# Optimization experiments

Hardware: AMD Instinct MI355X
Metric: run time of the kernel (lower is better)

## Reference

```python
import jax, jax.numpy as jnp
import numpy as np

B, C, VC, H, W = 4, 256, 128, 64, 64


def setup_inputs() -> dict:
    key = jax.random.key(0)
    kx, kq, kk, kv = jax.random.split(key, 4)
    # Conv2d 1x1 no-bias weights are just [out_channels, in_channels] matrices.
    s = 1.0 / np.sqrt(C)
    return {
        "x": jax.random.normal(kx, (B, C, H, W), dtype=jnp.float32),
        "Wq": jax.random.uniform(kq, (VC, C), minval=-s, maxval=s, dtype=jnp.float32),
        "Wk": jax.random.uniform(kk, (VC, C), minval=-s, maxval=s, dtype=jnp.float32),
        "Wv": jax.random.uniform(kv, (VC, C), minval=-s, maxval=s, dtype=jnp.float32),
    }


def reference(x, Wq, Wk, Wv):
    # 1x1 convs == per-pixel channel GEMMs
    Q = jnp.einsum('bchw,dc->bdhw', x, Wq)  # [B, VC, H, W]
    K = jnp.einsum('bchw,dc->bdhw', x, Wk)
    V = jnp.einsum('bchw,dc->bdhw', x, Wv)
    b, d, h, w = Q.shape
    # affinity over all spatial pairs: [B, H, W, H, W]
    aff = jnp.einsum('bdij,bdkl->bijkl', Q, K).reshape(b, h, w, h * w)
    aff = jax.nn.softmax(aff, axis=3).reshape(b, h, w, h, w)
    # attention-weighted aggregation of values
    out = jnp.einsum('bijkl,bdkl->bdij', aff, V)  # [B, VC, H, W]
    return out
```

## Files before the change

kernel.cpp:

```cpp
#include <hip/hip_runtime.h>
#include <hip/hip_bf16.h>

#define B_ 4
#define C_ 256
#define D_ 128
#define N_ 4096

typedef float f32x4 __attribute__((ext_vector_type(4)));
typedef short bf16x8 __attribute__((ext_vector_type(8)));
typedef short s16x4 __attribute__((ext_vector_type(4)));
typedef unsigned short u16;
typedef unsigned int u32;

__device__ __forceinline__ u16 f2bf(float f) {
  unsigned u = __float_as_uint(f);
  u += 0x7fffu + ((u >> 16) & 1u);
  return (u16)(u >> 16);
}
__device__ __forceinline__ float bf2f(u16 v) {
  return __uint_as_float(((u32)v) << 16);
}
__device__ __forceinline__ u32 cvt_pk_bf16(float a, float b) {
  u32 r;
  asm("v_cvt_pk_bf16_f32 %0, %1, %2" : "=v"(r) : "v"(a), "v"(b));
  return r;
}

__global__ __launch_bounds__(256) void castw_kernel(
    const float* __restrict__ Wq, const float* __restrict__ Wk,
    const float* __restrict__ Wv, u16* __restrict__ Whi,
    u16* __restrict__ Wlo) {
  const int i = blockIdx.x * 256 + threadIdx.x;
  const int m = i >> 13;
  const int j = (i & 8191) * 4;
  const float* src = (m == 0) ? Wq : (m == 1) ? Wk : Wv;
  const float scale = (m == 0) ? 1.44269504f : 1.0f;
  const float4 v = *(const float4*)(src + j);
  const float vv[4] = {v.x * scale, v.y * scale, v.z * scale, v.w * scale};
  s16x4 h, l;
#pragma unroll
  for (int k = 0; k < 4; ++k) {
    const u16 hb = f2bf(vv[k]);
    h[k] = (short)hb;
    l[k] = (short)f2bf(vv[k] - bf2f(hb));
  }
  *(s16x4*)&Whi[m * 32768 + j] = h;
  *(s16x4*)&Wlo[m * 32768 + j] = l;
}

__global__ __launch_bounds__(256, 2) void proj_kernel(
    const float* __restrict__ x, const u16* __restrict__ Whi,
    const u16* __restrict__ Wlo, u16* __restrict__ Qo, u16* __restrict__ Ko,
    u16* __restrict__ Vt) {
  __shared__ __align__(16) u16 xs_h[32 * 256];
  __shared__ __align__(16) u16 xs_l[32 * 256];

  const int n0 = blockIdx.x * 32;
  const int b = blockIdx.y;
  const int t = threadIdx.x;
  const int w = t >> 6, lane = t & 63, g = lane >> 4, c = lane & 15;

  {
    const float* xb = x + ((size_t)b * C_) * N_ + n0;
#pragma unroll
    for (int r = 0; r < 8; ++r) {
      const int id = r * 256 + t;
      const int cr = id >> 3, nq = (id & 7) * 4;
      const float4 v = *(const float4*)(xb + (size_t)cr * N_ + nq);
      const float vv[4] = {v.x, v.y, v.z, v.w};
#pragma unroll
      for (int k2 = 0; k2 < 4; ++k2) {
        const int idx2 = (nq + k2) * 256 + (cr ^ (((nq + k2) & 7) << 3));
        const u16 hb = f2bf(vv[k2]);
        xs_h[idx2] = hb;
        xs_l[idx2] = f2bf(vv[k2] - bf2f(hb));
      }
    }
  }
  __syncthreads();

  if (w < 2) {
    const size_t wo = (size_t)w * 32768;
    u16* __restrict__ O = (w == 0 ? Qo : Ko) + (size_t)b * N_ * D_;
#pragma unroll 1
    for (int dt = 0; dt < 8; ++dt) {
      bf16x8 wfh[8], wfl[8];
#pragma unroll
      for (int kc = 0; kc < 8; ++kc) {
        const size_t off = wo + (size_t)(dt * 16 + c) * 256 + kc * 32 + g * 8;
        wfh[kc] = *(const bf16x8*)&Whi[off];
        wfl[kc] = *(const bf16x8*)&Wlo[off];
      }
#pragma unroll
      for (int nt = 0; nt < 2; ++nt) {
        f32x4 a = {0.f, 0.f, 0.f, 0.f};
#pragma unroll
        for (int kc = 0; kc < 8; ++kc) {
          const int xi = (nt * 16 + c) * 256 +
                         ((kc * 32 + g * 8) ^ ((c & 7) << 3));
          const bf16x8 xh = *(const bf16x8*)&xs_h[xi];
          const bf16x8 xl = *(const bf16x8*)&xs_l[xi];
          a = __builtin_amdgcn_mfma_f32_16x16x32_bf16(xh, wfh[kc], a, 0, 0, 0);
          a = __builtin_amdgcn_mfma_f32_16x16x32_bf16(xh, wfl[kc], a, 0, 0, 0);
          a = __builtin_amdgcn_mfma_f32_16x16x32_bf16(xl, wfh[kc], a, 0, 0, 0);
        }
#pragma unroll
        for (int i = 0; i < 4; ++i)
          O[(size_t)(n0 + nt * 16 + g * 4 + i) * D_ + dt * 16 + c] = f2bf(a[i]);
      }
    }
  } else {
    const size_t wo = (size_t)2 * 32768;
    const int d0 = (w - 2) * 64;
    u16* __restrict__ O = Vt + (size_t)b * D_ * N_;
#pragma unroll 1
    for (int dt = 0; dt < 4; ++dt) {
      bf16x8 wfh[8], wfl[8];
#pragma unroll
      for (int kc = 0; kc < 8; ++kc) {
        const size_t off =
            wo + (size_t)(d0 + dt * 16 + c) * 256 + kc * 32 + g * 8;
        wfh[kc] = *(const bf16x8*)&Whi[off];
        wfl[kc] = *(const bf16x8*)&Wlo[off];
      }
#pragma unroll
      for (int nt = 0; nt < 2; ++nt) {
        f32x4 a = {0.f, 0.f, 0.f, 0.f};
#pragma unroll
        for (int kc = 0; kc < 8; ++kc) {
          const int xi = (nt * 16 + c) * 256 +
                         ((kc * 32 + g * 8) ^ ((c & 7) << 3));
          const bf16x8 xh = *(const bf16x8*)&xs_h[xi];
          const bf16x8 xl = *(const bf16x8*)&xs_l[xi];
          a = __builtin_amdgcn_mfma_f32_16x16x32_bf16(wfh[kc], xh, a, 0, 0, 0);
          a = __builtin_amdgcn_mfma_f32_16x16x32_bf16(wfl[kc], xh, a, 0, 0, 0);
          a = __builtin_amdgcn_mfma_f32_16x16x32_bf16(wfh[kc], xl, a, 0, 0, 0);
        }
#pragma unroll
        for (int i = 0; i < 4; ++i)
          O[(size_t)(d0 + dt * 16 + g * 4 + i) * N_ + n0 + nt * 16 + c] =
              f2bf(a[i]);
      }
    }
  }
}

__device__ __forceinline__ int kIdx(int row, int col) {
  return row * 128 + (col ^ ((row & 7) << 3));
}
__device__ __forceinline__ int vIdx(int d, int col) {
  return d * 64 + (col ^ ((d & 7) << 3));
}
__device__ __forceinline__ int pIdx(int q, int col) {
  return q * 64 + (col ^ ((q & 7) << 3));
}

__global__ __launch_bounds__(256, 2) void attn_kernel(
    const u16* __restrict__ Q, const u16* __restrict__ K,
    const u16* __restrict__ Vt, u16* __restrict__ op,
    float* __restrict__ mb, float* __restrict__ lb,
    float* __restrict__ outf, int qt, int rem) {
  __shared__ __align__(16) u16 lds_k[64 * 128];
  __shared__ __align__(16) u16 lds_vt[128 * 64];
  __shared__ __align__(16) u16 lds_p[4][32 * 64];

  const int b = blockIdx.y;
  const int sid = blockIdx.z;
  const int q0 = blockIdx.x * 128;
  const int NT = qt + (sid < rem ? 1 : 0);
  const int t0 = sid * qt + (sid < rem ? sid : rem);
  const int k0 = t0 * 64;
  const int t = threadIdx.x;
  const int w = t >> 6, lane = t & 63, g = lane >> 4, c = lane & 15;
  const int qw = q0 + w * 32;

  const u16* __restrict__ Qb = Q + (size_t)b * N_ * D_;
  const u16* __restrict__ Kb = K + (size_t)b * N_ * D_;
  const u16* __restrict__ Vb = Vt + (size_t)b * D_ * N_;

  bf16x8 qf[2][4];
#pragma unroll
  for (int qh = 0; qh < 2; ++qh)
#pragma unroll
    for (int kc = 0; kc < 4; ++kc)
      qf[qh][kc] =
          *(const bf16x8*)&Qb[(size_t)(qw + qh * 16 + c) * D_ + kc * 32 + g * 8];

  f32x4 acc[8][2];
#pragma unroll
  for (int dt = 0; dt < 8; ++dt)
#pragma unroll
    for (int qh = 0; qh < 2; ++qh) acc[dt][qh] = (f32x4){0.f, 0.f, 0.f, 0.f};
  float mrow[2] = {-3.0e38f, -3.0e38f};
  float lrow[2] = {0.f, 0.f};
  const float THR = 11.5415603f;

  bf16x8 krg[4], vrg[4];
  auto load_tile = [&](int kbase) {
#pragma unroll
    for (int i = 0; i < 4; ++i) {
      const int idx = i * 256 + t;
      krg[i] = *(const bf16x8*)&Kb[(size_t)(kbase + (idx >> 4)) * D_ + (idx & 15) * 8];
      vrg[i] = *(const bf16x8*)&Vb[(size_t)(idx >> 3) * N_ + kbase + (idx & 7) * 8];
    }
  };
  load_tile(k0);

  u16* __restrict__ pw = lds_p[w];

  for (int kt = 0; kt < NT; ++kt) {
    __syncthreads();
#pragma unroll
    for (int i = 0; i < 4; ++i) {
      const int idx = i * 256 + t;
      *(bf16x8*)&lds_k[kIdx(idx >> 4, (idx & 15) * 8)] = krg[i];
      *(bf16x8*)&lds_vt[vIdx(idx >> 3, (idx & 7) * 8)] = vrg[i];
    }
    if (kt + 1 < NT) load_tile(k0 + (kt + 1) * 64);
    __syncthreads();

    f32x4 s[4][2];
#pragma unroll
    for (int ct = 0; ct < 4; ++ct)
#pragma unroll
      for (int qh = 0; qh < 2; ++qh) s[ct][qh] = (f32x4){0.f, 0.f, 0.f, 0.f};
    __builtin_amdgcn_s_setprio(1);
#pragma unroll
    for (int kc = 0; kc < 4; ++kc) {
#pragma unroll
      for (int ct = 0; ct < 4; ++ct) {
        const bf16x8 kf =
            *(const bf16x8*)&lds_k[kIdx(ct * 16 + c, kc * 32 + g * 8)];
        s[ct][0] = __builtin_amdgcn_mfma_f32_16x16x32_bf16(kf, qf[0][kc], s[ct][0], 0, 0, 0);
        s[ct][1] = __builtin_amdgcn_mfma_f32_16x16x32_bf16(kf, qf[1][kc], s[ct][1], 0, 0, 0);
      }
    }
    __builtin_amdgcn_s_setprio(0);

    float pm[2];
#pragma unroll
    for (int qh = 0; qh < 2; ++qh) {
      const float m0 = fmaxf(fmaxf(s[0][qh][0], s[0][qh][1]),
                             fmaxf(s[0][qh][2], s[0][qh][3]));
      const float m1 = fmaxf(fmaxf(s[1][qh][0], s[1][qh][1]),
                             fmaxf(s[1][qh][2], s[1][qh][3]));
      const float m2 = fmaxf(fmaxf(s[2][qh][0], s[2][qh][1]),
                             fmaxf(s[2][qh][2], s[2][qh][3]));
      const float m3 = fmaxf(fmaxf(s[3][qh][0], s[3][qh][1]),
                             fmaxf(s[3][qh][2], s[3][qh][3]));
      float p = fmaxf(fmaxf(m0, m1), fmaxf(m2, m3));
      p = fmaxf(p, __shfl_xor(p, 16));
      p = fmaxf(p, __shfl_xor(p, 32));
      pm[qh] = p;
    }
    const bool need =
        __any((pm[0] > mrow[0] + THR) || (pm[1] > mrow[1] + THR));
    if (need) {
#pragma unroll
      for (int qh = 0; qh < 2; ++qh) {
        const float mnew = fmaxf(mrow[qh], pm[qh]);
        const float scl = exp2f(mrow[qh] - mnew);
        lrow[qh] *= scl;
        mrow[qh] = mnew;
#pragma unroll
        for (int dt = 0; dt < 8; ++dt) {
          acc[dt][qh][0] *= scl; acc[dt][qh][1] *= scl;
          acc[dt][qh][2] *= scl; acc[dt][qh][3] *= scl;
        }
      }
    }
#pragma unroll
    for (int qh = 0; qh < 2; ++qh) {
      float rs = 0.f;
#pragma unroll
      for (int ct = 0; ct < 4; ++ct)
#pragma unroll
        for (int i = 0; i < 4; ++i) {
          const float p = exp2f(s[ct][qh][i] - mrow[qh]);
          s[ct][qh][i] = p;
          rs += p;
        }
      rs += __shfl_xor(rs, 16);
      rs += __shfl_xor(rs, 32);
      lrow[qh] += rs;
    }

#pragma unroll
    for (int qh = 0; qh < 2; ++qh)
#pragma unroll
      for (int ct = 0; ct < 4; ++ct) {
        const int pi = pIdx(qh * 16 + c, ct * 16 + g * 4);
        union { u32 w2[2]; s16x4 v; } pu;
        pu.w2[0] = cvt_pk_bf16(s[ct][qh][0], s[ct][qh][1]);
        pu.w2[1] = cvt_pk_bf16(s[ct][qh][2], s[ct][qh][3]);
        *(s16x4*)&pw[pi] = pu.v;
      }
    asm volatile("" ::: "memory");

    __builtin_amdgcn_s_setprio(1);
#pragma unroll
    for (int kc = 0; kc < 2; ++kc) {
      const bf16x8 pf0 = *(const bf16x8*)&pw[pIdx(c, kc * 32 + g * 8)];
      const bf16x8 pf1 = *(const bf16x8*)&pw[pIdx(16 + c, kc * 32 + g * 8)];
#pragma unroll
      for (int dt = 0; dt < 8; ++dt) {
        const bf16x8 vf =
            *(const bf16x8*)&lds_vt[vIdx(dt * 16 + c, kc * 32 + g * 8)];
        acc[dt][0] = __builtin_amdgcn_mfma_f32_16x16x32_bf16(vf, pf0, acc[dt][0], 0, 0, 0);
        acc[dt][1] = __builtin_amdgcn_mfma_f32_16x16x32_bf16(vf, pf1, acc[dt][1], 0, 0, 0);
      }
    }
    __builtin_amdgcn_s_setprio(0);
  }

#pragma unroll
  for (int qh = 0; qh < 2; ++qh) {
    const int n = qw + qh * 16 + c;
    if (mb) {
      u16* __restrict__ ob = op + ((size_t)(sid * B_ + b) * D_) * N_;
#pragma unroll
      for (int dt = 0; dt < 8; ++dt)
#pragma unroll
        for (int i = 0; i < 4; ++i)
          ob[(size_t)(dt * 16 + g * 4 + i) * N_ + n] = f2bf(acc[dt][qh][i]);
      if (g == 0) {
        mb[(size_t)(sid * B_ + b) * N_ + n] = mrow[qh];
        lb[(size_t)(sid * B_ + b) * N_ + n] = lrow[qh];
      }
    } else {
      const float linv = 1.0f / lrow[qh];
      float* __restrict__ ob = outf + (size_t)b * D_ * N_;
#pragma unroll
      for (int dt = 0; dt < 8; ++dt)
#pragma unroll
        for (int i = 0; i < 4; ++i)
          ob[(size_t)(dt * 16 + g * 4 + i) * N_ + n] = acc[dt][qh][i] * linv;
    }
  }
}

__global__ __launch_bounds__(256) void combine_kernel(
    const u16* __restrict__ op, const float* __restrict__ mbu,
    const float* __restrict__ lbu, float* __restrict__ out, int S) {
  const int idx = blockIdx.x * 256 + threadIdx.x;
  const int n0 = (idx & (N_ / 4 - 1)) * 4;
  const int bd = idx >> 10;
  const int b = bd >> 7, d = bd & (D_ - 1);

  float4 msv[8], lsv[8];
  float M0 = -3e38f, M1 = -3e38f, M2 = -3e38f, M3 = -3e38f;
#pragma unroll
  for (int s = 0; s < 8; ++s)
    if (s < S) {
      msv[s] = *(const float4*)&mbu[(size_t)(s * B_ + b) * N_ + n0];
      lsv[s] = *(const float4*)&lbu[(size_t)(s * B_ + b) * N_ + n0];
      M0 = fmaxf(M0, msv[s].x); M1 = fmaxf(M1, msv[s].y);
      M2 = fmaxf(M2, msv[s].z); M3 = fmaxf(M3, msv[s].w);
    }
  float d0 = 0.f, d1 = 0.f, d2 = 0.f, d3 = 0.f;
  float a0 = 0.f, a1 = 0.f, a2 = 0.f, a3 = 0.f;
#pragma unroll
  for (int s = 0; s < 8; ++s)
    if (s < S) {
      const float w0 = exp2f(msv[s].x - M0);
      const float w1 = exp2f(msv[s].y - M1);
      const float w2 = exp2f(msv[s].z - M2);
      const float w3 = exp2f(msv[s].w - M3);
      d0 += lsv[s].x * w0; d1 += lsv[s].y * w1;
      d2 += lsv[s].z * w2; d3 += lsv[s].w * w3;
      const s16x4 o =
          *(const s16x4*)&op[((size_t)(s * B_ + b) * D_ + d) * N_ + n0];
      a0 += w0 * bf2f((u16)o[0]); a1 += w1 * bf2f((u16)o[1]);
      a2 += w2 * bf2f((u16)o[2]); a3 += w3 * bf2f((u16)o[3]);
    }
  float4 r = {a0 / d0, a1 / d1, a2 / d2, a3 / d3};
  *(float4*)&out[((size_t)b * D_ + d) * N_ + n0] = r;
}

extern "C" void kernel_launch(void* const* d_in, const int* in_sizes, int n_in,
                              void* d_out, int out_size, void* d_ws, size_t ws_size,
                              hipStream_t stream) {
  const float* x  = (const float*)d_in[0];
  const float* Wq = (const float*)d_in[1];
  const float* Wk = (const float*)d_in[2];
  const float* Wv = (const float*)d_in[3];
  float* out = (float*)d_out;

  u16* whi  = (u16*)d_ws;
  u16* wlo  = whi + (size_t)3 * 128 * 256;
  u16* q_ws = wlo + (size_t)3 * 128 * 256;
  u16* k_ws = q_ws + (size_t)B_ * N_ * D_;
  u16* v_ws = k_ws + (size_t)B_ * N_ * D_;

  castw_kernel<<<96, 256, 0, stream>>>(Wq, Wk, Wv, whi, wlo);
  proj_kernel<<<dim3(N_ / 32, B_), 256, 0, stream>>>(x, whi, wlo, q_ws, k_ws,
                                                     v_ws);

  const size_t baseB =
      ((size_t)6 * 128 * 256 + (size_t)3 * B_ * N_ * D_) * 2;
  int S = 0;
  const int cands[4] = {6, 4, 2, 1};
  for (int ci = 0; ci < 4; ++ci) {
    const int cand = cands[ci];
    const size_t need = baseB + (size_t)cand * ((size_t)B_ * D_ * N_ * 2 +
                                                (size_t)2 * B_ * N_ * 4);
    if (ws_size >= need) { S = cand; break; }
  }
  if (S > 1) {
    u16* opb = (u16*)((char*)d_ws + baseB);
    float* mbuf = (float*)(opb + (size_t)S * B_ * D_ * N_);
    float* lbuf = mbuf + (size_t)S * B_ * N_;
    attn_kernel<<<dim3(N_ / 128, B_, S), 256, 0, stream>>>(
        q_ws, k_ws, v_ws, opb, mbuf, lbuf, nullptr, 64 / S, 64 % S);
    combine_kernel<<<(B_ * D_ * N_ / 4) / 256, 256, 0, stream>>>(opb, mbuf,
                                                                 lbuf, out, S);
  } else {
    attn_kernel<<<dim3(N_ / 128, B_, 1), 256, 0, stream>>>(
        q_ws, k_ws, v_ws, nullptr, nullptr, nullptr, out, 64, 0);
  }
}
```

Baseline: 103.2 us.

## Keep softmax probabilities in registers via lane shuffles and permuted V layout

Drops the per-wave LDS staging buffer for the bf16 probability tile. The S accumulator fragments are converted in registers and exchanged across lanes with xor-32 shuffles to form the PV MFMA B operand. The V tile is now written to LDS with a matching k-permutation so the reduction order still lines up. This removes LDS round-trips and frees shared memory, at the cost of extra shuffles, selects and split 8-byte V stores.

```diff
diff --git a/kernel.cpp b/kernel.cpp
--- a/kernel.cpp
+++ b/kernel.cpp
@@ -151,8 +151,10 @@
 __device__ __forceinline__ int vIdx(int d, int col) {
   return d * 64 + (col ^ ((d & 7) << 3));
 }
-__device__ __forceinline__ int pIdx(int q, int col) {
-  return q * 64 + (col ^ ((q & 7) << 3));
+__device__ __forceinline__ int kprm(int q) {
+  const int ct = q >> 2, qq = q & 3;
+  return ((ct >> 1) << 5) +
+         (((qq >> 1) == (ct & 1)) ? (qq << 3) : (((qq ^ 2) << 3) + 4));
 }
 
 __global__ __launch_bounds__(256, 2) void attn_kernel(
@@ -162,7 +164,6 @@
     float* __restrict__ outf, int qt, int rem) {
   __shared__ __align__(16) u16 lds_k[64 * 128];
   __shared__ __align__(16) u16 lds_vt[128 * 64];
-  __shared__ __align__(16) u16 lds_p[4][32 * 64];
 
   const int b = blockIdx.y;
   const int sid = blockIdx.z;
@@ -173,6 +174,7 @@
   const int t = threadIdx.x;
   const int w = t >> 6, lane = t & 63, g = lane >> 4, c = lane & 15;
   const int qw = q0 + w * 32;
+  const bool ghi = (g & 2) != 0;
 
   const u16* __restrict__ Qb = Q + (size_t)b * N_ * D_;
   const u16* __restrict__ Kb = K + (size_t)b * N_ * D_;
@@ -206,15 +208,18 @@
   };
   load_tile(k0);
 
-  u16* __restrict__ pw = lds_p[w];
-
   for (int kt = 0; kt < NT; ++kt) {
     __syncthreads();
 #pragma unroll
     for (int i = 0; i < 4; ++i) {
       const int idx = i * 256 + t;
       *(bf16x8*)&lds_k[kIdx(idx >> 4, (idx & 15) * 8)] = krg[i];
-      *(bf16x8*)&lds_vt[vIdx(idx >> 3, (idx & 7) * 8)] = vrg[i];
+      const int d = idx >> 3, rc = idx & 7;
+      s16x4 lo, hi;
+      lo[0] = vrg[i][0]; lo[1] = vrg[i][1]; lo[2] = vrg[i][2]; lo[3] = vrg[i][3];
+      hi[0] = vrg[i][4]; hi[1] = vrg[i][5]; hi[2] = vrg[i][6]; hi[3] = vrg[i][7];
+      *(s16x4*)&lds_vt[vIdx(d, kprm(rc * 2))] = lo;
+      *(s16x4*)&lds_vt[vIdx(d, kprm(rc * 2 + 1))] = hi;
     }
     if (kt + 1 < NT) load_tile(k0 + (kt + 1) * 64);
     __syncthreads();
@@ -285,32 +290,39 @@
       lrow[qh] += rs;
     }
 
-#pragma unroll
-    for (int qh = 0; qh < 2; ++qh)
-#pragma unroll
-      for (int ct = 0; ct < 4; ++ct) {
-        const int pi = pIdx(qh * 16 + c, ct * 16 + g * 4);
-        union { u32 w2[2]; s16x4 v; } pu;
-        pu.w2[0] = cvt_pk_bf16(s[ct][qh][0], s[ct][qh][1]);
-        pu.w2[1] = cvt_pk_bf16(s[ct][qh][2], s[ct][qh][3]);
-        *(s16x4*)&pw[pi] = pu.v;
-      }
-    asm volatile("" ::: "memory");
-
-    __builtin_amdgcn_s_setprio(1);
+    u32 pfw[2][2][4];
 #pragma unroll
     for (int kc = 0; kc < 2; ++kc) {
-      const bf16x8 pf0 = *(const bf16x8*)&pw[pIdx(c, kc * 32 + g * 8)];
-      const bf16x8 pf1 = *(const bf16x8*)&pw[pIdx(16 + c, kc * 32 + g * 8)];
+#pragma unroll
+      for (int qh = 0; qh < 2; ++qh) {
+        const u32 lo0 = cvt_pk_bf16(s[kc * 2][qh][0], s[kc * 2][qh][1]);
+        const u32 lo1 = cvt_pk_bf16(s[kc * 2][qh][2], s[kc * 2][qh][3]);
+        const u32 hi0 = cvt_pk_bf16(s[kc * 2 + 1][qh][0], s[kc * 2 + 1][qh][1]);
+        const u32 hi1 = cvt_pk_bf16(s[kc * 2 + 1][qh][2], s[kc * 2 + 1][qh][3]);
+        pfw[kc][qh][0] = ghi ? hi0 : lo0;
+        pfw[kc][qh][1] = ghi ? hi1 : lo1;
+        const u32 s0 = ghi ? lo0 : hi0;
+        const u32 s1 = ghi ? lo1 : hi1;
+        pfw[kc][qh][2] = (u32)__shfl_xor((int)s0, 32);
+        pfw[kc][qh][3] = (u32)__shfl_xor((int)s1, 32);
+      }
+    }
+
+#pragma unroll
+    for (int kc = 0; kc < 2; ++kc) {
+      union { u32 w[4]; bf16x8 v; } u0, u1;
+#pragma unroll
+      for (int j = 0; j < 4; ++j) { u0.w[j] = pfw[kc][0][j]; u1.w[j] = pfw[kc][1][j]; }
+      __builtin_amdgcn_s_setprio(1);
 #pragma unroll
       for (int dt = 0; dt < 8; ++dt) {
         const bf16x8 vf =
             *(const bf16x8*)&lds_vt[vIdx(dt * 16 + c, kc * 32 + g * 8)];
-        acc[dt][0] = __builtin_amdgcn_mfma_f32_16x16x32_bf16(vf, pf0, acc[dt][0], 0, 0, 0);
-        acc[dt][1] = __builtin_amdgcn_mfma_f32_16x16x32_bf16(vf, pf1, acc[dt][1], 0, 0, 0);
-      }
-    }
-    __builtin_amdgcn_s_setprio(0);
+        acc[dt][0] = __builtin_amdgcn_mfma_f32_16x16x32_bf16(vf, u0.v, acc[dt][0], 0, 0, 0);
+        acc[dt][1] = __builtin_amdgcn_mfma_f32_16x16x32_bf16(vf, u1.v, acc[dt][1], 0, 0, 0);
+      }
+      __builtin_amdgcn_s_setprio(0);
+    }
   }
 
 #pragma unroll
```

Measured after the change: 103.2 us. No clear change (-0.0%).
